# Kernel tuning notes

Hardware: AMD Instinct MI355X
Metric: run time of the kernel (lower is better)

Reference implementation:

```python
import jax, jax.numpy as jnp
import numpy as np

N = 8192
D = 2048      # input_dim
DH = 1024     # input_dim // r
DO = 1024     # output_dim

def setup_inputs() -> dict:
    key = jax.random.key(0)
    ks = jax.random.split(key, 11)
    s_in = 1.0 / np.sqrt(D)
    s_h = 1.0 / np.sqrt(DH)
    return {
        "O0": jax.random.normal(ks[0], (N, D), dtype=jnp.float32),
        "Ww": jax.random.uniform(ks[1], (DH, D), jnp.float32, -s_in, s_in),
        "Wb": jax.random.uniform(ks[2], (DH,), jnp.float32, -s_in, s_in),
        "Uw": jax.random.uniform(ks[3], (DH, D), jnp.float32, -s_in, s_in),
        "Ub": jax.random.uniform(ks[4], (DH,), jnp.float32, -s_in, s_in),
        "Hw": jax.random.uniform(ks[5], (DH, D), jnp.float32, -s_in, s_in),
        "Hb": jax.random.uniform(ks[6], (DH,), jnp.float32, -s_in, s_in),
        "fc0w": jax.random.uniform(ks[7], (D, DH), jnp.float32, -s_h, s_h),
        "fc0b": jax.random.uniform(ks[8], (D,), jnp.float32, -s_h, s_h),
        "fc1w": jax.random.uniform(ks[9], (DO, D), jnp.float32, -s_in, s_in),
        "fc1b": jax.random.uniform(ks[10], (DO,), jnp.float32, -s_in, s_in),
    }

def reference(O0, Ww, Wb, Uw, Ub, Hw, Hb, fc0w, fc0b, fc1w, fc1b):
    q = O0 @ Ww.T + Wb              # [N, DH]
    k = O0 @ Uw.T + Ub              # [N, DH]
    v = O0 @ Hw.T + Hb              # [N, DH]
    scores = q @ k.T                # [N, N], unscaled as in the original
    R1 = jax.nn.softmax(scores, axis=1)
    ctx = R1 @ v                    # [N, DH]
    O1 = O0 + (ctx @ fc0w.T + fc0b) # residual, [N, D]
    O2 = O1 @ fc1w.T + fc1b         # [N, DO]
    return (O1, O2)
```

## Files before the change

kernel.cpp:

```cpp
#include <hip/hip_runtime.h>
#include <cstdint>
#include <cstddef>

typedef _Float16 f16;
typedef _Float16 f16x8 __attribute__((ext_vector_type(8)));
typedef _Float16 f16x4 __attribute__((ext_vector_type(4)));
typedef float    f32x4 __attribute__((ext_vector_type(4)));

#define BM 128
#define BN 128
#define BK 64

__global__ __launch_bounds__(256) void cvt_f32_f16(const float* __restrict__ in,
                                                   f16* __restrict__ out, int n) {
  int i = (blockIdx.x * 256 + threadIdx.x) * 4;
  if (i < n) {
    float4 v = *(const float4*)(in + i);
    f16x4 h; h[0] = (f16)v.x; h[1] = (f16)v.y; h[2] = (f16)v.z; h[3] = (f16)v.w;
    *(f16x4*)(out + i) = h;
  }
}

__global__ __launch_bounds__(256) void transpose_f16(const f16* __restrict__ in,
                                                     int ldi,
                                                     f16* __restrict__ out,
                                                     int R, int C) {
  __shared__ f16 tile[64][65];
  const int r0 = blockIdx.y * 64, c0 = blockIdx.x * 64;
  const int t = threadIdx.x;
#pragma unroll
  for (int p = 0; p < 2; p++) {
    int s = t + p * 256;
    int r = s >> 3, q = s & 7;
    f16x8 v = *(const f16x8*)(in + (size_t)(r0 + r) * ldi + c0 + q * 8);
#pragma unroll
    for (int e = 0; e < 8; e++) tile[r][q * 8 + e] = v[e];
  }
  __syncthreads();
#pragma unroll
  for (int p = 0; p < 2; p++) {
    int s = t + p * 256;
    int r = s >> 3, q = s & 7;
    f16x8 v;
#pragma unroll
    for (int e = 0; e < 8; e++) v[e] = tile[q * 8 + e][r];
    *(f16x8*)(out + (size_t)(c0 + r) * R + r0 + q * 8) = v;
  }
}

template <int MODE>
__global__ __launch_bounds__(256) void gemm_bt(
    const f16* __restrict__ A, const f16* __restrict__ B,
    int M, int N, int K, int lda, int ldb,
    const float* __restrict__ bias,
    f16* __restrict__ outH, int ldo,
    float* __restrict__ stats, int sld,
    const float* __restrict__ resid, int ldr,
    float* __restrict__ outF, int ldof) {
  __shared__ f16 lA[BM * BK];
  __shared__ f16 lB[BN * BK];
  const int t = threadIdx.x;
  const int m0 = blockIdx.y * BM, n0 = blockIdx.x * BN;
  const int wave = t >> 6, lane = t & 63;
  const int wr = wave >> 1, wc = wave & 1;
  const int quad = lane >> 4, l16 = lane & 15;

  const int rc = lane >> 3;
  const int kcs = (lane & 7) ^ rc;
  const uint32_t offA = (uint32_t)(rc * lda + kcs * 8) * 2u;
  const uint32_t offB = (uint32_t)(rc * ldb + kcs * 8) * 2u;
  const char* bAp = (const char*)(A + (size_t)m0 * lda);
  const char* bBp = (const char*)(B + (size_t)n0 * ldb);
  const int wq = __builtin_amdgcn_readfirstlane(wave * 4);

  f32x4 acc[4][4];
#pragma unroll
  for (int i = 0; i < 4; i++)
#pragma unroll
    for (int j = 0; j < 4; j++)
#pragma unroll
      for (int e = 0; e < 4; e++) acc[i][j][e] = 0.0f;

  const int nk = K / BK;
  for (int kt = 0; kt < nk; ++kt) {
    const size_t kb = (size_t)(kt * BK) * 2;
#pragma unroll
    for (int j = 0; j < 4; j++) {
      const int c = wq + j;
      __builtin_amdgcn_global_load_lds(
          (const __attribute__((address_space(1))) void*)
              (bAp + ((size_t)(c * 8) * lda * 2 + kb) + offA),
          (__attribute__((address_space(3))) void*)(lA + c * 512), 16, 0, 0);
      __builtin_amdgcn_global_load_lds(
          (const __attribute__((address_space(1))) void*)
              (bBp + ((size_t)(c * 8) * ldb * 2 + kb) + offB),
          (__attribute__((address_space(3))) void*)(lB + c * 512), 16, 0, 0);
    }
    __syncthreads();

    f16x8 af[2][4], bf[2][4];
#pragma unroll
    for (int h = 0; h < 2; h++) {
      const int p = ((h * 4 + quad) ^ (l16 & 7)) * 8;
#pragma unroll
      for (int i = 0; i < 4; i++)
        af[h][i] = *(const f16x8*)(lA + (wr * 64 + i * 16 + l16) * 64 + p);
#pragma unroll
      for (int j = 0; j < 4; j++)
        bf[h][j] = *(const f16x8*)(lB + (wc * 64 + j * 16 + l16) * 64 + p);
    }
#pragma unroll
    for (int h = 0; h < 2; h++)
#pragma unroll
      for (int i = 0; i < 4; i++)
#pragma unroll
        for (int j = 0; j < 4; j++)
          acc[i][j] = __builtin_amdgcn_mfma_f32_16x16x32_f16(af[h][i], bf[h][j],
                                                             acc[i][j], 0, 0, 0);
    __syncthreads();
  }

  const int mrow = m0 + wr * 64;
  const int ncol = n0 + wc * 64;
  float bv[4];
  if constexpr (MODE == 0 || MODE == 3 || MODE == 4) {
#pragma unroll
    for (int j = 0; j < 4; j++) bv[j] = bias[ncol + j * 16 + l16];
  }
#pragma unroll
  for (int fi = 0; fi < 4; fi++) {
#pragma unroll
    for (int i = 0; i < 4; i++) {
      const int gr = mrow + fi * 16 + quad * 4 + i;
      if constexpr (MODE == 1) {
        float mx = fmaxf(fmaxf(acc[fi][0][i], acc[fi][1][i]),
                         fmaxf(acc[fi][2][i], acc[fi][3][i]));
        mx = fmaxf(mx, __shfl_xor(mx, 1));
        mx = fmaxf(mx, __shfl_xor(mx, 2));
        mx = fmaxf(mx, __shfl_xor(mx, 4));
        mx = fmaxf(mx, __shfl_xor(mx, 8));
        if (l16 == 0) stats[(size_t)gr * sld + (blockIdx.x * 2 + wc)] = mx;
        f16* rp = outH + (size_t)gr * ldo + ncol + l16;
        rp[0]  = (f16)(acc[fi][0][i] - mx);
        rp[16] = (f16)(acc[fi][1][i] - mx);
        rp[32] = (f16)(acc[fi][2][i] - mx);
        rp[48] = (f16)(acc[fi][3][i] - mx);
      } else if constexpr (MODE == 0) {
        f16* rp = outH + (size_t)gr * ldo + ncol + l16;
        rp[0]  = (f16)(acc[fi][0][i] + bv[0]);
        rp[16] = (f16)(acc[fi][1][i] + bv[1]);
        rp[32] = (f16)(acc[fi][2][i] + bv[2]);
        rp[48] = (f16)(acc[fi][3][i] + bv[3]);
      } else if constexpr (MODE == 2) {
        f16* rp = outH + (size_t)gr * ldo + ncol + l16;
        rp[0]  = (f16)acc[fi][0][i];
        rp[16] = (f16)acc[fi][1][i];
        rp[32] = (f16)acc[fi][2][i];
        rp[48] = (f16)acc[fi][3][i];
      } else if constexpr (MODE == 3) {
        float* rf = outF + (size_t)gr * ldof + ncol + l16;
        const float* rr = resid + (size_t)gr * ldr + ncol + l16;
        f16* rh = outH + (size_t)gr * ldo + ncol + l16;
        float o0 = acc[fi][0][i] + bv[0] + rr[0];
        float o1 = acc[fi][1][i] + bv[1] + rr[16];
        float o2 = acc[fi][2][i] + bv[2] + rr[32];
        float o3 = acc[fi][3][i] + bv[3] + rr[48];
        rf[0] = o0; rf[16] = o1; rf[32] = o2; rf[48] = o3;
        rh[0] = (f16)o0; rh[16] = (f16)o1; rh[32] = (f16)o2; rh[48] = (f16)o3;
      } else {
        float* rf = outF + (size_t)gr * ldof + ncol + l16;
        rf[0]  = acc[fi][0][i] + bv[0];
        rf[16] = acc[fi][1][i] + bv[1];
        rf[32] = acc[fi][2][i] + bv[2];
        rf[48] = acc[fi][3][i] + bv[3];
      }
    }
  }
}

__global__ __launch_bounds__(256) void softmax_row(f16* __restrict__ S,
                                                   const float* __restrict__ stats,
                                                   int N, int sld) {
  const int row = blockIdx.x;
  const int t = threadIdx.x;
  __shared__ float sm[128];
  __shared__ float red[4];
  if (t < 128) sm[t] = stats[(size_t)row * sld + t];
  __syncthreads();
  float m = -1e30f;
#pragma unroll 16
  for (int i = 0; i < 128; i++) m = fmaxf(m, sm[i]);

  f16* rp = S + (size_t)row * N + t * 32;
  const float d = sm[t >> 1] - m;
  float ev[32];
  float sum = 0.0f;
#pragma unroll
  for (int v8 = 0; v8 < 4; v8++) {
    f16x8 v = *(f16x8*)(rp + v8 * 8);
#pragma unroll
    for (int e = 0; e < 8; e++) {
      float x = (float)v[e] + d;
      float ex = __expf(x);
      ev[v8 * 8 + e] = ex;
      sum += ex;
    }
  }
#pragma unroll
  for (int off = 32; off > 0; off >>= 1) sum += __shfl_down(sum, off);
  if ((t & 63) == 0) red[t >> 6] = sum;
  __syncthreads();
  const float rl = 1.0f / (red[0] + red[1] + red[2] + red[3]);
#pragma unroll
  for (int v8 = 0; v8 < 4; v8++) {
    f16x8 v;
#pragma unroll
    for (int e = 0; e < 8; e++) v[e] = (f16)(ev[v8 * 8 + e] * rl);
    *(f16x8*)(rp + v8 * 8) = v;
  }
}

extern "C" void kernel_launch(void* const* d_in, const int* in_sizes, int n_in,
                              void* d_out, int out_size, void* d_ws, size_t ws_size,
                              hipStream_t stream) {
  const float* O0   = (const float*)d_in[0];
  const float* Ww   = (const float*)d_in[1];
  const float* Wb   = (const float*)d_in[2];
  const float* Uw   = (const float*)d_in[3];
  const float* Ub   = (const float*)d_in[4];
  const float* Hw   = (const float*)d_in[5];
  const float* Hb   = (const float*)d_in[6];
  const float* fc0w = (const float*)d_in[7];
  const float* fc0b = (const float*)d_in[8];
  const float* fc1w = (const float*)d_in[9];
  const float* fc1b = (const float*)d_in[10];

  const int N = 8192, D = 2048, DH = 1024, DO = 1024;
  const int NQKV = 3 * DH;

  char* w = (char*)d_ws;
  f16* Wwh   = (f16*)w; w += (size_t)DH * D * 2;
  f16* Uwh   = (f16*)w; w += (size_t)DH * D * 2;
  f16* Hwh   = (f16*)w; w += (size_t)DH * D * 2;
  f16* fc0wh = (f16*)w; w += (size_t)D * DH * 2;
  f16* fc1wh = (f16*)w; w += (size_t)DO * D * 2;
  f16* ctxh  = (f16*)w; w += (size_t)N * DH * 2;
  float* stats = (float*)w; w += (size_t)N * 128 * 4;
  float* biasC = (float*)w; w += (size_t)NQKV * 4;
  w = (char*)(((uintptr_t)w + 255) & ~(uintptr_t)255);
  f16* Sb    = (f16*)w;

  f16* oh   = (f16*)d_out;
  f16* qkv  = oh;
  f16* qh   = qkv;
  f16* kh   = qkv + DH;
  f16* vh   = qkv + 2 * DH;
  f16* O0h  = oh + (size_t)N * NQKV;
  f16* vT   = O0h + (size_t)N * D;
  f16* O1h  = Sb;

  {
    int n = DH * D;
    int grid = n / 1024;
    cvt_f32_f16<<<grid, 256, 0, stream>>>(Ww, Wwh, n);
    cvt_f32_f16<<<grid, 256, 0, stream>>>(Uw, Uwh, n);
    cvt_f32_f16<<<grid, 256, 0, stream>>>(Hw, Hwh, n);
    cvt_f32_f16<<<grid, 256, 0, stream>>>(fc0w, fc0wh, n);
    cvt_f32_f16<<<grid, 256, 0, stream>>>(fc1w, fc1wh, n);
    cvt_f32_f16<<<(N * D) / 1024, 256, 0, stream>>>(O0, O0h, N * D);
    hipMemcpyAsync(biasC,          Wb, DH * 4, hipMemcpyDeviceToDevice, stream);
    hipMemcpyAsync(biasC + DH,     Ub, DH * 4, hipMemcpyDeviceToDevice, stream);
    hipMemcpyAsync(biasC + 2 * DH, Hb, DH * 4, hipMemcpyDeviceToDevice, stream);
  }

  gemm_bt<0><<<dim3(NQKV / BN, N / BM), 256, 0, stream>>>(
      O0h, Wwh, N, NQKV, D, D, D, biasC,
      qkv, NQKV, nullptr, 0, nullptr, 0, nullptr, 0);

  transpose_f16<<<dim3(DH / 64, N / 64), 256, 0, stream>>>(vh, NQKV, vT, N, DH);

  gemm_bt<1><<<dim3(N / BN, N / BM), 256, 0, stream>>>(
      qh, kh, N, N, DH, NQKV, NQKV, nullptr, Sb, N, stats, 128,
      nullptr, 0, nullptr, 0);

  softmax_row<<<N, 256, 0, stream>>>(Sb, stats, N, 128);

  gemm_bt<2><<<dim3(DH / BN, N / BM), 256, 0, stream>>>(
      Sb, vT, N, DH, N, N, N, nullptr, ctxh, DH, nullptr, 0, nullptr, 0,
      nullptr, 0);

  gemm_bt<3><<<dim3(D / BN, N / BM), 256, 0, stream>>>(
      ctxh, fc0wh, N, D, DH, DH, DH, fc0b, O1h, D, nullptr, 0,
      O0, D, (float*)d_out, D);

  gemm_bt<4><<<dim3(DO / BN, N / BM), 256, 0, stream>>>(
      O1h, fc1wh, N, DO, D, D, D, fc1b, nullptr, 0, nullptr, 0,
      nullptr, 0, (float*)d_out + (size_t)N * D, DO);
}
```

Measured before the change: 862.9 us.

## Fuse softmax exp into score GEMM and rescale per-tile in PV GEMM

The score GEMM epilogue now computes exp relative to each 64-column tile's local max and writes per-tile max and sum statistics. A small kernel merges those statistics into per-row, per-tile scale factors (stored transposed). The PV GEMM multiplies the A fragments by these factors on the fly. This removes the separate full read-modify-write pass over the 8192x8192 fp16 score matrix. The cost is extra exp work in the GEMM epilogue, per-k-tile alpha loads and fp16 multiplies in the PV GEMM, and some precision risk from scaling in fp16.

```diff
diff --git a/kernel.cpp b/kernel.cpp
--- a/kernel.cpp
+++ b/kernel.cpp
@@ -54,7 +54,8 @@
     int M, int N, int K, int lda, int ldb,
     const float* __restrict__ bias,
     f16* __restrict__ outH, int ldo,
-    float* __restrict__ stats, int sld,
+    float* __restrict__ statsM, float* __restrict__ statsS, int sld,
+    const float* __restrict__ alphaT,
     const float* __restrict__ resid, int ldr,
     float* __restrict__ outF, int ldof) {
   __shared__ f16 lA[BM * BK];
@@ -83,6 +84,11 @@
 
   const int nk = K / BK;
   for (int kt = 0; kt < nk; ++kt) {
+    float al[4];
+    if constexpr (MODE == 2) {
+      const float* ap = alphaT + (size_t)kt * M + m0 + wr * 64 + l16;
+      al[0] = ap[0]; al[1] = ap[16]; al[2] = ap[32]; al[3] = ap[48];
+    }
     const size_t kb = (size_t)(kt * BK) * 2;
 #pragma unroll
     for (int j = 0; j < 4; j++) {
@@ -109,6 +115,14 @@
       for (int j = 0; j < 4; j++)
         bf[h][j] = *(const f16x8*)(lB + (wc * 64 + j * 16 + l16) * 64 + p);
     }
+    if constexpr (MODE == 2) {
+#pragma unroll
+      for (int i = 0; i < 4; i++) {
+        const f16 ah = (f16)al[i];
+        af[0][i] = af[0][i] * ah;
+        af[1][i] = af[1][i] * ah;
+      }
+    }
 #pragma unroll
     for (int h = 0; h < 2; h++)
 #pragma unroll
@@ -139,12 +153,24 @@
         mx = fmaxf(mx, __shfl_xor(mx, 2));
         mx = fmaxf(mx, __shfl_xor(mx, 4));
         mx = fmaxf(mx, __shfl_xor(mx, 8));
-        if (l16 == 0) stats[(size_t)gr * sld + (blockIdx.x * 2 + wc)] = mx;
+        float e0 = __expf(acc[fi][0][i] - mx);
+        float e1 = __expf(acc[fi][1][i] - mx);
+        float e2 = __expf(acc[fi][2][i] - mx);
+        float e3 = __expf(acc[fi][3][i] - mx);
+        float sm = (e0 + e1) + (e2 + e3);
+        sm += __shfl_xor(sm, 1);
+        sm += __shfl_xor(sm, 2);
+        sm += __shfl_xor(sm, 4);
+        sm += __shfl_xor(sm, 8);
+        if (l16 == 0) {
+          statsM[(size_t)gr * sld + (blockIdx.x * 2 + wc)] = mx;
+          statsS[(size_t)gr * sld + (blockIdx.x * 2 + wc)] = sm;
+        }
         f16* rp = outH + (size_t)gr * ldo + ncol + l16;
-        rp[0]  = (f16)(acc[fi][0][i] - mx);
-        rp[16] = (f16)(acc[fi][1][i] - mx);
-        rp[32] = (f16)(acc[fi][2][i] - mx);
-        rp[48] = (f16)(acc[fi][3][i] - mx);
+        rp[0]  = (f16)e0;
+        rp[16] = (f16)e1;
+        rp[32] = (f16)e2;
+        rp[48] = (f16)e3;
       } else if constexpr (MODE == 0) {
         f16* rp = outH + (size_t)gr * ldo + ncol + l16;
         rp[0]  = (f16)(acc[fi][0][i] + bv[0]);
@@ -178,45 +204,39 @@
   }
 }
 
-__global__ __launch_bounds__(256) void softmax_row(f16* __restrict__ S,
-                                                   const float* __restrict__ stats,
-                                                   int N, int sld) {
-  const int row = blockIdx.x;
+__global__ __launch_bounds__(256) void alpha_from_stats(
+    const float* __restrict__ sM, const float* __restrict__ sS,
+    float* __restrict__ aT, int rows) {
+  __shared__ float alph[128][65];
   const int t = threadIdx.x;
-  __shared__ float sm[128];
-  __shared__ float red[4];
-  if (t < 128) sm[t] = stats[(size_t)row * sld + t];
-  __syncthreads();
-  float m = -1e30f;
-#pragma unroll 16
-  for (int i = 0; i < 128; i++) m = fmaxf(m, sm[i]);
-
-  f16* rp = S + (size_t)row * N + t * 32;
-  const float d = sm[t >> 1] - m;
+  const int r = t >> 2, j = t & 3;
+  const int row = blockIdx.x * 64 + r;
+  const float* pm = sM + (size_t)row * 128 + j * 32;
+  const float* ps = sS + (size_t)row * 128 + j * 32;
+  float mv[32];
+  float mx = -1e30f;
+#pragma unroll
+  for (int c = 0; c < 32; c++) { mv[c] = pm[c]; mx = fmaxf(mx, mv[c]); }
+  mx = fmaxf(mx, __shfl_xor(mx, 1));
+  mx = fmaxf(mx, __shfl_xor(mx, 2));
   float ev[32];
   float sum = 0.0f;
 #pragma unroll
-  for (int v8 = 0; v8 < 4; v8++) {
-    f16x8 v = *(f16x8*)(rp + v8 * 8);
-#pragma unroll
-    for (int e = 0; e < 8; e++) {
-      float x = (float)v[e] + d;
-      float ex = __expf(x);
-      ev[v8 * 8 + e] = ex;
-      sum += ex;
-    }
-  }
-#pragma unroll
-  for (int off = 32; off > 0; off >>= 1) sum += __shfl_down(sum, off);
-  if ((t & 63) == 0) red[t >> 6] = sum;
+  for (int c = 0; c < 32; c++) {
+    ev[c] = __expf(mv[c] - mx);
+    sum += ev[c] * ps[c];
+  }
+  sum += __shfl_xor(sum, 1);
+  sum += __shfl_xor(sum, 2);
+  const float rl = 1.0f / sum;
+#pragma unroll
+  for (int c = 0; c < 32; c++) alph[j * 32 + c][r] = ev[c] * rl;
   __syncthreads();
-  const float rl = 1.0f / (red[0] + red[1] + red[2] + red[3]);
-#pragma unroll
-  for (int v8 = 0; v8 < 4; v8++) {
-    f16x8 v;
-#pragma unroll
-    for (int e = 0; e < 8; e++) v[e] = (f16)(ev[v8 * 8 + e] * rl);
-    *(f16x8*)(rp + v8 * 8) = v;
+  const int wid = t >> 6, rr = t & 63;
+#pragma unroll
+  for (int c = 0; c < 32; c++) {
+    const int tg = c * 4 + wid;
+    aT[(size_t)tg * rows + blockIdx.x * 64 + rr] = alph[tg][rr];
   }
 }
 
@@ -244,11 +264,14 @@
   f16* Hwh   = (f16*)w; w += (size_t)DH * D * 2;
   f16* fc0wh = (f16*)w; w += (size_t)D * DH * 2;
   f16* fc1wh = (f16*)w; w += (size_t)DO * D * 2;
-  f16* ctxh  = (f16*)w; w += (size_t)N * DH * 2;
-  float* stats = (float*)w; w += (size_t)N * 128 * 4;
+  float* aT  = (float*)w; w += (size_t)128 * N * 4;
+  char* un = w; w += (size_t)N * DH * 2;
+  float* statsM = (float*)un;
+  float* statsS = statsM + (size_t)N * 128;
+  f16* ctxh = (f16*)un;
   float* biasC = (float*)w; w += (size_t)NQKV * 4;
   w = (char*)(((uintptr_t)w + 255) & ~(uintptr_t)255);
-  f16* Sb    = (f16*)w;
+  f16* Sb = (f16*)w;
 
   f16* oh   = (f16*)d_out;
   f16* qkv  = oh;
@@ -275,25 +298,26 @@
 
   gemm_bt<0><<<dim3(NQKV / BN, N / BM), 256, 0, stream>>>(
       O0h, Wwh, N, NQKV, D, D, D, biasC,
-      qkv, NQKV, nullptr, 0, nullptr, 0, nullptr, 0);
+      qkv, NQKV, nullptr, nullptr, 0, nullptr, nullptr, 0, nullptr, 0);
 
   transpose_f16<<<dim3(DH / 64, N / 64), 256, 0, stream>>>(vh, NQKV, vT, N, DH);
 
   gemm_bt<1><<<dim3(N / BN, N / BM), 256, 0, stream>>>(
-      qh, kh, N, N, DH, NQKV, NQKV, nullptr, Sb, N, stats, 128,
-      nullptr, 0, nullptr, 0);
-
-  softmax_row<<<N, 256, 0, stream>>>(Sb, stats, N, 128);
+      qh, kh, N, N, DH, NQKV, NQKV, nullptr, Sb, N,
+      statsM, statsS, 128, nullptr, nullptr, 0, nullptr, 0);
+
+  alpha_from_stats<<<N / 64, 256, 0, stream>>>(statsM, statsS, aT, N);
 
   gemm_bt<2><<<dim3(DH / BN, N / BM), 256, 0, stream>>>(
-      Sb, vT, N, DH, N, N, N, nullptr, ctxh, DH, nullptr, 0, nullptr, 0,
-      nullptr, 0);
+      Sb, vT, N, DH, N, N, N, nullptr, ctxh, DH,
+      nullptr, nullptr, 0, aT, nullptr, 0, nullptr, 0);
 
   gemm_bt<3><<<dim3(D / BN, N / BM), 256, 0, stream>>>(
-      ctxh, fc0wh, N, D, DH, DH, DH, fc0b, O1h, D, nullptr, 0,
-      O0, D, (float*)d_out, D);
+      ctxh, fc0wh, N, D, DH, DH, DH, fc0b, O1h, D,
+      nullptr, nullptr, 0, nullptr, O0, D, (float*)d_out, D);
 
   gemm_bt<4><<<dim3(DO / BN, N / BM), 256, 0, stream>>>(
-      O1h, fc1wh, N, DO, D, D, D, fc1b, nullptr, 0, nullptr, 0,
-      nullptr, 0, (float*)d_out + (size_t)N * D, DO);
-}
+      O1h, fc1wh, N, DO, D, D, D, fc1b, nullptr, 0,
+      nullptr, nullptr, 0, nullptr, nullptr, 0,
+      (float*)d_out + (size_t)N * D, DO);
+}
```

Measured after the change: 855.6 us. Within noise of the previous version (-0.8%).
